# Kernel optimization log

Measured on AMD Instinct MI355X. Metric: run time of the kernel, lower is better.

Reference implementation:

```python
import jax, jax.numpy as jnp
import numpy as np

NUM_HEADS = 16

def setup_inputs() -> dict:
    key = jax.random.key(0)
    k1, k2, k3, k4 = jax.random.split(key, 4)
    B, S, E = 4, 2048, 1024
    return {
        "q": jax.random.normal(k1, (B, S, E), dtype=jnp.float32),
        "k": jax.random.normal(k2, (B, S, E), dtype=jnp.float32),
        "v": jax.random.normal(k3, (B, S, E), dtype=jnp.float32),
        "w_out": jax.random.normal(k4, (E, E), dtype=jnp.float32) * (E ** -0.5),
        "b_out": jnp.zeros((E,), dtype=jnp.float32),
    }

def reference(q, k, v, w_out, b_out):
    B, S, E = q.shape
    H = NUM_HEADS
    D = E // H
    scale = D ** -0.5
    # split heads: [B, S, E] -> [B, H, S, D]
    def split(x):
        return x.reshape(B, S, H, D).transpose(0, 2, 1, 3)
    qh, kh, vh = split(q), split(k), split(v)
    scores = jnp.einsum('bhqd,bhkd->bhqk', qh, kh) * scale  # [B,H,S,S]
    weights = jax.nn.softmax(scores, axis=-1)
    # dropout is identity in eval mode
    out = jnp.einsum('bhqk,bhkd->bhqd', weights, vh)
    out = out.transpose(0, 2, 1, 3).reshape(B, S, E)  # merge heads
    return out @ w_out.T + b_out
```

## Files before the change

kernel.cpp:

```cpp
#include <hip/hip_runtime.h>
#include <cstdint>
#include <cstddef>

typedef __attribute__((ext_vector_type(8))) short bf16x8;
typedef __attribute__((ext_vector_type(4))) float f32x4;
typedef __attribute__((ext_vector_type(16))) float f32x16;

#define MFMA16(a, b, c) __builtin_amdgcn_mfma_f32_16x16x32_bf16((a), (b), (c), 0, 0, 0)
#define MFMA32(a, b, c) __builtin_amdgcn_mfma_f32_32x32x16_bf16((a), (b), (c), 0, 0, 0)

constexpr int Bz = 4, S = 2048, E = 1024, H = 16, Dh = 64;
constexpr size_t BSE = (size_t)Bz * S * E;

__device__ __forceinline__ unsigned short f2bf(float f) {
    uint32_t u = __builtin_bit_cast(uint32_t, f);
    u += 0x7FFFu + ((u >> 16) & 1u);
    return (unsigned short)(u >> 16);
}

__device__ __forceinline__ float exp2_fast(float x) {
#if __has_builtin(__builtin_amdgcn_exp2f)
    return __builtin_amdgcn_exp2f(x);
#else
    return exp2f(x);
#endif
}

__device__ __forceinline__ uint32_t pack_bf16(float a, float b) {
    uint32_t ua = __builtin_bit_cast(uint32_t, a) + 0x8000u;
    uint32_t ub = __builtin_bit_cast(uint32_t, b) + 0x8000u;
#if __has_builtin(__builtin_amdgcn_perm)
    return __builtin_amdgcn_perm(ub, ua, 0x07060302u);
#else
    return (ua >> 16) | (ub & 0xFFFF0000u);
#endif
}

__device__ __forceinline__ void gload16(const unsigned short* g, unsigned short* l) {
    __builtin_amdgcn_global_load_lds((const __attribute__((address_space(1))) void*)g,
                                     (__attribute__((address_space(3))) void*)l, 16, 0, 0);
}

__global__ __launch_bounds__(256) void convert_kernel(const float* __restrict__ in,
                                                      unsigned short* __restrict__ out,
                                                      int n4) {
    int i = blockIdx.x * blockDim.x + threadIdx.x;
    if (i < n4) {
        float4 f = ((const float4*)in)[i];
        uint2 u;
        u.x = pack_bf16(f.x, f.y);
        u.y = pack_bf16(f.z, f.w);
        ((uint2*)out)[i] = u;
    }
}

__global__ __launch_bounds__(256) void prep_kv(const float* __restrict__ k,
                                               const float* __restrict__ v,
                                               unsigned short* __restrict__ kb,
                                               unsigned short* __restrict__ vt) {
    __shared__ unsigned short tile[64][65];
    const int b = blockIdx.z, h = blockIdx.y, s0 = blockIdx.x * 64;
    const int r = threadIdx.x >> 2, cb = (threadIdx.x & 3) * 16;
    const size_t off = (size_t)(b * S + s0 + r) * E + h * Dh + cb;

    {
        const float* src = k + off;
        uint32_t o[8];
#pragma unroll
        for (int j = 0; j < 8; ++j) {
            float2 f = *(const float2*)(src + 2 * j);
            o[j] = pack_bf16(f.x, f.y);
        }
        unsigned short* dst = kb + off;
        *(uint4*)(dst) = *(const uint4*)(o);
        *(uint4*)(dst + 8) = *(const uint4*)(o + 4);
    }
    {
        const float* src = v + off;
#pragma unroll
        for (int j = 0; j < 16; j += 4) {
            float4 f = *(const float4*)(src + j);
            tile[cb + j + 0][r] = f2bf(f.x);
            tile[cb + j + 1][r] = f2bf(f.y);
            tile[cb + j + 2][r] = f2bf(f.z);
            tile[cb + j + 3][r] = f2bf(f.w);
        }
    }
    __syncthreads();
    const int dv = threadIdx.x >> 2, seg = (threadIdx.x & 3) * 16;
    unsigned short* dst = vt + (((size_t)(b * H + h) * Dh + dv) * S + s0 + seg);
    *(uint4*)(dst) = *(const uint4*)(&tile[dv][seg]);
    *(uint4*)(dst + 8) = *(const uint4*)(&tile[dv][seg] + 8);
}

constexpr int GSTR = 528;
__global__ __launch_bounds__(256, 2) void attn_kernel(const float* __restrict__ q,
                                                      const unsigned short* __restrict__ kb,
                                                      const unsigned short* __restrict__ vt,
                                                      unsigned short* __restrict__ attn) {
    __shared__ unsigned short smem[18432];

    const int wid = blockIdx.x + 8 * (blockIdx.y + 16 * blockIdx.z);
    const int c_ = wid & 7, j_ = wid >> 3;
    const int bh = c_ * 8 + (j_ >> 3), qblk = j_ & 7;
    const int b = bh >> 4, h = bh & 15;

    const int tid = threadIdx.x;
    const int wave = tid >> 6, lane = tid & 63;
    const int l32 = lane & 31, half = lane >> 5;
    const int x7 = l32 & 7, y4 = l32 >> 3;

    const int q0 = qblk * 256 + wave * 64;
    const float scl = 0.125f * 1.44269504088896f;

    bf16x8 qreg[2][4];
#pragma unroll
    for (int qh = 0; qh < 2; ++qh) {
        const float* qsrc = q + ((size_t)(b * S + q0 + qh * 32 + l32)) * E + h * Dh + half * 8;
#pragma unroll
        for (int t = 0; t < 4; ++t) {
            float4 f0 = *(const float4*)(qsrc + 16 * t);
            float4 f1 = *(const float4*)(qsrc + 16 * t + 4);
            bf16x8 r;
            r[0] = (short)f2bf(f0.x * scl); r[1] = (short)f2bf(f0.y * scl);
            r[2] = (short)f2bf(f0.z * scl); r[3] = (short)f2bf(f0.w * scl);
            r[4] = (short)f2bf(f1.x * scl); r[5] = (short)f2bf(f1.y * scl);
            r[6] = (short)f2bf(f1.z * scl); r[7] = (short)f2bf(f1.w * scl);
            qreg[qh][t] = r;
        }
    }

    f32x16 fzero;
#pragma unroll
    for (int r = 0; r < 16; ++r) fzero[r] = 0.f;
    f32x16 oacc[2][2];
#pragma unroll
    for (int qh = 0; qh < 2; ++qh)
#pragma unroll
        for (int mt = 0; mt < 2; ++mt) oacc[qh][mt] = fzero;
    float lsum[2] = {0.f, 0.f};

    const int row8 = lane >> 3;
    const int sg = (lane & 7) ^ row8;
    const unsigned short* kbase = kb + ((size_t)(b * S)) * E + h * Dh;
    const unsigned short* vtb = vt + ((size_t)(b * H + h) * Dh) * S;

    auto stage = [&](int kt, int bsel) {
        unsigned short* ksb = smem + bsel * 8448;
        unsigned short* vsb = ksb + 4224;
#pragma unroll
        for (int u = 0; u < 2; ++u) {
            const int gi = wave * 2 + u;
            gload16(kbase + (size_t)(kt * 64 + gi * 8 + row8) * E + sg * 8, ksb + gi * GSTR);
            gload16(vtb + (size_t)(gi * 8 + row8) * S + kt * 64 + sg * 8, vsb + gi * GSTR);
        }
    };

    int roff[2];
#pragma unroll
    for (int mt = 0; mt < 2; ++mt) roff[mt] = (mt * 4 + y4) * GSTR + x7 * 64;

    constexpr int NT = S / 64;
    stage(0, 0);

    for (int kt = 0; kt < NT; ++kt) {
        const int cur = kt & 1;
        __syncthreads();
        if (kt + 1 < NT) stage(kt + 1, cur ^ 1);
        const unsigned short* ksb = smem + cur * 8448;
        const unsigned short* vsb = ksb + 4224;

        bf16x8 kfrag[2][4];
#pragma unroll
        for (int mt = 0; mt < 2; ++mt)
#pragma unroll
            for (int t = 0; t < 4; ++t)
                kfrag[mt][t] = *(const bf16x8*)(ksb + roff[mt] + (((t * 2 + half) ^ x7) * 8));

        f32x16 st[2][2];
#pragma unroll
        for (int qh = 0; qh < 2; ++qh)
#pragma unroll
            for (int mt = 0; mt < 2; ++mt) {
                st[qh][mt] = MFMA32(kfrag[mt][0], qreg[qh][0], fzero);
#pragma unroll
                for (int t = 1; t < 4; ++t)
                    st[qh][mt] = MFMA32(kfrag[mt][t], qreg[qh][t], st[qh][mt]);
            }

        uint32_t pkd[2][2][4][2];
#pragma unroll
        for (int qh = 0; qh < 2; ++qh) {
            float ls = 0.f;
#pragma unroll
            for (int mt = 0; mt < 2; ++mt)
#pragma unroll
                for (int g = 0; g < 4; ++g) {
                    float p0 = exp2_fast(st[qh][mt][4 * g + 0]);
                    float p1 = exp2_fast(st[qh][mt][4 * g + 1]);
                    float p2 = exp2_fast(st[qh][mt][4 * g + 2]);
                    float p3 = exp2_fast(st[qh][mt][4 * g + 3]);
                    ls += (p0 + p1) + (p2 + p3);
                    pkd[qh][mt][g][0] = pack_bf16(p0, p1);
                    pkd[qh][mt][g][1] = pack_bf16(p2, p3);
                }
            lsum[qh] += ls;
        }

        bf16x8 vfrag[2][4];
#pragma unroll
        for (int mt = 0; mt < 2; ++mt)
#pragma unroll
            for (int c = 0; c < 4; ++c)
                vfrag[mt][c] = *(const bf16x8*)(vsb + roff[mt] + (((c * 2 + half) ^ x7) * 8));

#pragma unroll
        for (int qh = 0; qh < 2; ++qh)
#pragma unroll
            for (int c = 0; c < 4; ++c) {
                const int ms = c >> 1;
                const int g0 = 2 * (c & 1);
                uint32_t a0 = pkd[qh][ms][g0][0], a1 = pkd[qh][ms][g0][1];
                uint32_t b0 = pkd[qh][ms][g0 + 1][0], b1 = pkd[qh][ms][g0 + 1][1];
                uint32_t snd0 = half ? a0 : b0;
                uint32_t snd1 = half ? a1 : b1;
                uint32_t r0 = (uint32_t)__shfl_xor((int)snd0, 32);
                uint32_t r1 = (uint32_t)__shfl_xor((int)snd1, 32);
                int4 bi;
                bi.x = (int)(half ? r0 : a0);
                bi.y = (int)(half ? r1 : a1);
                bi.z = (int)(half ? b0 : r0);
                bi.w = (int)(half ? b1 : r1);
                bf16x8 bfrag = __builtin_bit_cast(bf16x8, bi);
#pragma unroll
                for (int mt = 0; mt < 2; ++mt)
                    oacc[qh][mt] = MFMA32(vfrag[mt][c], bfrag, oacc[qh][mt]);
            }
    }

    __syncthreads();
    float inv[2];
#pragma unroll
    for (int qh = 0; qh < 2; ++qh) {
        float l = lsum[qh] + (float)__shfl_xor(lsum[qh], 32);
        inv[qh] = 1.0f / l;
    }

    unsigned short* ob = smem + wave * (64 * 72);
#pragma unroll
    for (int qh = 0; qh < 2; ++qh)
#pragma unroll
        for (int mt = 0; mt < 2; ++mt)
#pragma unroll
            for (int g = 0; g < 4; ++g) {
                int dv0 = 8 * g + 4 * half + 32 * mt;
                uint2 w2;
                w2.x = pack_bf16(oacc[qh][mt][4 * g + 0] * inv[qh],
                                 oacc[qh][mt][4 * g + 1] * inv[qh]);
                w2.y = pack_bf16(oacc[qh][mt][4 * g + 2] * inv[qh],
                                 oacc[qh][mt][4 * g + 3] * inv[qh]);
                *(uint2*)(ob + (qh * 32 + l32) * 72 + dv0) = w2;
            }
    __syncthreads();
#pragma unroll
    for (int it = 0; it < 2; ++it) {
        int row = it * 32 + (lane >> 1);
        int seg = (lane & 1) * 32;
        unsigned short* gdst = attn + ((size_t)(b * S + q0 + row)) * E + h * Dh + seg;
#pragma unroll
        for (int j = 0; j < 4; ++j) {
            bf16x8 v8 = *(const bf16x8*)(ob + row * 72 + seg + j * 8);
            *(bf16x8*)(gdst + j * 8) = v8;
        }
    }
}

__global__ __launch_bounds__(256) void proj_kernel(const unsigned short* __restrict__ A,
                                                   const unsigned short* __restrict__ W,
                                                   const float* __restrict__ bias,
                                                   float* __restrict__ C) {
    __shared__ unsigned short smem[16384];
    const int tid = threadIdx.x;
    const int wave = tid >> 6, lane = tid & 63, quad = lane >> 4, l16 = lane & 15;
    const int wm = wave >> 1, wn = wave & 1;
    const int m0 = blockIdx.x * 128, n0 = blockIdx.y * 128;

    f32x4 acc[4][4];
    f32x4 zero = {0.f, 0.f, 0.f, 0.f};
#pragma unroll
    for (int mi = 0; mi < 4; ++mi)
#pragma unroll
        for (int ni = 0; ni < 4; ++ni) acc[mi][ni] = zero;

    const int row16 = lane >> 2, slot = lane & 3;
    const unsigned short* Abase = A + (size_t)m0 * 1024;
    const unsigned short* Wbase = W + (size_t)n0 * 1024;

    auto stage = [&](int k0, int bsel) {
        unsigned short* as = smem + bsel * 8192;
        unsigned short* bs = as + 4096;
#pragma unroll
        for (int i = 0; i < 2; ++i) {
            const int g = wave * 2 + i;
            const int r = g * 16 + row16;
            gload16(Abase + (size_t)r * 1024 + k0 + slot * 8, as + g * 512);
            gload16(Wbase + (size_t)r * 1024 + k0 + slot * 8, bs + g * 512);
        }
    };

    constexpr int NT = 1024 / 32;
    stage(0, 0);

    for (int t = 0; t < NT; ++t) {
        const int cur = t & 1;
        __syncthreads();
        if (t + 1 < NT) stage((t + 1) * 32, cur ^ 1);
        const unsigned short* as = smem + cur * 8192;
        const unsigned short* bs = as + 4096;

        bf16x8 af[4], bfr[4];
#pragma unroll
        for (int mi = 0; mi < 4; ++mi)
            af[mi] = *(const bf16x8*)(as + (wm * 64 + mi * 16 + l16) * 32 + quad * 8);
#pragma unroll
        for (int ni = 0; ni < 4; ++ni)
            bfr[ni] = *(const bf16x8*)(bs + (wn * 64 + ni * 16 + l16) * 32 + quad * 8);
#pragma unroll
        for (int mi = 0; mi < 4; ++mi)
#pragma unroll
            for (int ni = 0; ni < 4; ++ni)
                acc[mi][ni] = MFMA16(af[mi], bfr[ni], acc[mi][ni]);
    }

    float bb[4];
#pragma unroll
    for (int ni = 0; ni < 4; ++ni) bb[ni] = bias[n0 + wn * 64 + ni * 16 + l16];
#pragma unroll
    for (int mi = 0; mi < 4; ++mi) {
        const int row = m0 + wm * 64 + mi * 16 + quad * 4;
#pragma unroll
        for (int ni = 0; ni < 4; ++ni) {
            const int col = n0 + wn * 64 + ni * 16 + l16;
#pragma unroll
            for (int r = 0; r < 4; ++r)
                C[(size_t)(row + r) * 1024 + col] = acc[mi][ni][r] + bb[ni];
        }
    }
}

extern "C" void kernel_launch(void* const* d_in, const int* in_sizes, int n_in,
                              void* d_out, int out_size, void* d_ws, size_t ws_size,
                              hipStream_t stream) {
    const float* q = (const float*)d_in[0];
    const float* k = (const float*)d_in[1];
    const float* v = (const float*)d_in[2];
    const float* w = (const float*)d_in[3];
    const float* bias = (const float*)d_in[4];
    float* out = (float*)d_out;

    unsigned short* ws = (unsigned short*)d_ws;
    unsigned short* kb = ws;
    unsigned short* vt = kb + BSE;
    unsigned short* attnb = vt + BSE;
    unsigned short* wb = attnb + BSE;

    prep_kv<<<dim3(S / 64, H, Bz), dim3(256), 0, stream>>>(k, v, kb, vt);
    {
        int nw4 = (int)((size_t)E * E / 4);
        convert_kernel<<<dim3((nw4 + 255) / 256), dim3(256), 0, stream>>>(w, wb, nw4);
    }
    attn_kernel<<<dim3(S / 256, H, Bz), dim3(256), 0, stream>>>(q, kb, vt, attnb);
    proj_kernel<<<dim3((Bz * S) / 128, E / 128), dim3(256), 0, stream>>>(attnb, wb, bias, out);
}
```

Before: 252.7 us.

## Shrink projection tiles to 64x128, add MFMA priority hints, use RN bf16 packing

The output projection GEMM moves from 128x128 to 64x128 tiles on a 1D grid whose block index runs over N fastest, so neighbouring blocks share the same A rows. This doubles the block count to 1024 and cuts LDS use, aiming for better CU occupancy and load balance, at the cost of lower per-block data reuse. In the attention kernel, s_setprio raises wave priority around the MFMA sections to encourage overlap between waves. The fast bias-add bf16 packing of probabilities and outputs is also replaced with the library round-to-nearest-even conversion, which may add a few instructions per pack.

Result: slower. 273.2 us (+8.1%).

```diff
diff --git a/kernel.cpp b/kernel.cpp
--- a/kernel.cpp
+++ b/kernel.cpp
@@ -1,4 +1,5 @@
 #include <hip/hip_runtime.h>
+#include <hip/hip_bf16.h>
 #include <cstdint>
 #include <cstddef>
 
@@ -34,6 +35,16 @@
 #else
     return (ua >> 16) | (ub & 0xFFFF0000u);
 #endif
+}
+
+__device__ __forceinline__ uint32_t pack_bf16_rn(float a, float b) {
+    float2 f;
+    f.x = a;
+    f.y = b;
+    __hip_bfloat162 h = __float22bfloat162_rn(f);
+    uint32_t u;
+    __builtin_memcpy(&u, &h, 4);
+    return u;
 }
 
 __device__ __forceinline__ void gload16(const unsigned short* g, unsigned short* l) {
@@ -178,6 +189,7 @@
                 kfrag[mt][t] = *(const bf16x8*)(ksb + roff[mt] + (((t * 2 + half) ^ x7) * 8));
 
         f32x16 st[2][2];
+        __builtin_amdgcn_s_setprio(1);
 #pragma unroll
         for (int qh = 0; qh < 2; ++qh)
 #pragma unroll
@@ -187,6 +199,7 @@
                 for (int t = 1; t < 4; ++t)
                     st[qh][mt] = MFMA32(kfrag[mt][t], qreg[qh][t], st[qh][mt]);
             }
+        __builtin_amdgcn_s_setprio(0);
 
         uint32_t pkd[2][2][4][2];
 #pragma unroll
@@ -201,8 +214,8 @@
                     float p2 = exp2_fast(st[qh][mt][4 * g + 2]);
                     float p3 = exp2_fast(st[qh][mt][4 * g + 3]);
                     ls += (p0 + p1) + (p2 + p3);
-                    pkd[qh][mt][g][0] = pack_bf16(p0, p1);
-                    pkd[qh][mt][g][1] = pack_bf16(p2, p3);
+                    pkd[qh][mt][g][0] = pack_bf16_rn(p0, p1);
+                    pkd[qh][mt][g][1] = pack_bf16_rn(p2, p3);
                 }
             lsum[qh] += ls;
         }
@@ -232,9 +245,11 @@
                 bi.z = (int)(half ? b0 : r0);
                 bi.w = (int)(half ? b1 : r1);
                 bf16x8 bfrag = __builtin_bit_cast(bf16x8, bi);
+                __builtin_amdgcn_s_setprio(1);
 #pragma unroll
                 for (int mt = 0; mt < 2; ++mt)
                     oacc[qh][mt] = MFMA32(vfrag[mt][c], bfrag, oacc[qh][mt]);
+                __builtin_amdgcn_s_setprio(0);
             }
     }
 
@@ -255,10 +270,10 @@
             for (int g = 0; g < 4; ++g) {
                 int dv0 = 8 * g + 4 * half + 32 * mt;
                 uint2 w2;
-                w2.x = pack_bf16(oacc[qh][mt][4 * g + 0] * inv[qh],
-                                 oacc[qh][mt][4 * g + 1] * inv[qh]);
-                w2.y = pack_bf16(oacc[qh][mt][4 * g + 2] * inv[qh],
-                                 oacc[qh][mt][4 * g + 3] * inv[qh]);
+                w2.x = pack_bf16_rn(oacc[qh][mt][4 * g + 0] * inv[qh],
+                                    oacc[qh][mt][4 * g + 1] * inv[qh]);
+                w2.y = pack_bf16_rn(oacc[qh][mt][4 * g + 2] * inv[qh],
+                                    oacc[qh][mt][4 * g + 3] * inv[qh]);
                 *(uint2*)(ob + (qh * 32 + l32) * 72 + dv0) = w2;
             }
     __syncthreads();
@@ -279,16 +294,18 @@
                                                    const unsigned short* __restrict__ W,
                                                    const float* __restrict__ bias,
                                                    float* __restrict__ C) {
-    __shared__ unsigned short smem[16384];
+    __shared__ unsigned short smem[12288];
     const int tid = threadIdx.x;
     const int wave = tid >> 6, lane = tid & 63, quad = lane >> 4, l16 = lane & 15;
     const int wm = wave >> 1, wn = wave & 1;
-    const int m0 = blockIdx.x * 128, n0 = blockIdx.y * 128;
-
-    f32x4 acc[4][4];
+    const int id = blockIdx.x;
+    const int n0 = (id & 7) * 128;
+    const int m0 = (id >> 3) * 64;
+
+    f32x4 acc[2][4];
     f32x4 zero = {0.f, 0.f, 0.f, 0.f};
 #pragma unroll
-    for (int mi = 0; mi < 4; ++mi)
+    for (int mi = 0; mi < 2; ++mi)
 #pragma unroll
         for (int ni = 0; ni < 4; ++ni) acc[mi][ni] = zero;
 
@@ -297,15 +314,12 @@
     const unsigned short* Wbase = W + (size_t)n0 * 1024;
 
     auto stage = [&](int k0, int bsel) {
-        unsigned short* as = smem + bsel * 8192;
-        unsigned short* bs = as + 4096;
-#pragma unroll
-        for (int i = 0; i < 2; ++i) {
-            const int g = wave * 2 + i;
-            const int r = g * 16 + row16;
-            gload16(Abase + (size_t)r * 1024 + k0 + slot * 8, as + g * 512);
-            gload16(Wbase + (size_t)r * 1024 + k0 + slot * 8, bs + g * 512);
-        }
+        unsigned short* as = smem + bsel * 6144;
+        unsigned short* bs = as + 2048;
+        gload16(Abase + (size_t)(wave * 16 + row16) * 1024 + k0 + slot * 8, as + wave * 512);
+        gload16(Wbase + (size_t)(wave * 32 + row16) * 1024 + k0 + slot * 8, bs + wave * 1024);
+        gload16(Wbase + (size_t)(wave * 32 + 16 + row16) * 1024 + k0 + slot * 8,
+                bs + wave * 1024 + 512);
     };
 
     constexpr int NT = 1024 / 32;
@@ -315,18 +329,18 @@
         const int cur = t & 1;
         __syncthreads();
         if (t + 1 < NT) stage((t + 1) * 32, cur ^ 1);
-        const unsigned short* as = smem + cur * 8192;
-        const unsigned short* bs = as + 4096;
-
-        bf16x8 af[4], bfr[4];
-#pragma unroll
-        for (int mi = 0; mi < 4; ++mi)
-            af[mi] = *(const bf16x8*)(as + (wm * 64 + mi * 16 + l16) * 32 + quad * 8);
+        const unsigned short* as = smem + cur * 6144;
+        const unsigned short* bs = as + 2048;
+
+        bf16x8 af[2], bfr[4];
+#pragma unroll
+        for (int mi = 0; mi < 2; ++mi)
+            af[mi] = *(const bf16x8*)(as + (wm * 32 + mi * 16 + l16) * 32 + quad * 8);
 #pragma unroll
         for (int ni = 0; ni < 4; ++ni)
             bfr[ni] = *(const bf16x8*)(bs + (wn * 64 + ni * 16 + l16) * 32 + quad * 8);
 #pragma unroll
-        for (int mi = 0; mi < 4; ++mi)
+        for (int mi = 0; mi < 2; ++mi)
 #pragma unroll
             for (int ni = 0; ni < 4; ++ni)
                 acc[mi][ni] = MFMA16(af[mi], bfr[ni], acc[mi][ni]);
@@ -336,8 +350,8 @@
 #pragma unroll
     for (int ni = 0; ni < 4; ++ni) bb[ni] = bias[n0 + wn * 64 + ni * 16 + l16];
 #pragma unroll
-    for (int mi = 0; mi < 4; ++mi) {
-        const int row = m0 + wm * 64 + mi * 16 + quad * 4;
+    for (int mi = 0; mi < 2; ++mi) {
+        const int row = m0 + wm * 32 + mi * 16 + quad * 4;
 #pragma unroll
         for (int ni = 0; ni < 4; ++ni) {
             const int col = n0 + wn * 64 + ni * 16 + l16;
@@ -370,5 +384,5 @@
         convert_kernel<<<dim3((nw4 + 255) / 256), dim3(256), 0, stream>>>(w, wb, nw4);
     }
     attn_kernel<<<dim3(S / 256, H, Bz), dim3(256), 0, stream>>>(q, kb, vt, attnb);
-    proj_kernel<<<dim3((Bz * S) / 128, E / 128), dim3(256), 0, stream>>>(attnb, wb, bias, out);
-}
+    proj_kernel<<<dim3((Bz * S) / 64 * 8, 1), dim3(256), 0, stream>>>(attnb, wb, bias, out);
+}
```
